# Kernel optimization log

Measured on AMD Instinct MI355X. Metric: run time of the kernel, lower is better.

## Reference

```python
import jax, jax.numpy as jnp
import numpy as np

B, S, D, A = 16, 2048, 512, 512

def setup_inputs() -> dict:
    key = jax.random.key(0)
    ks = jax.random.split(key, 7)
    scale = 1.0 / np.sqrt(D)
    return {
        "query": jax.random.normal(ks[0], (B, S, D), dtype=jnp.float32),
        "key_": jax.random.normal(ks[1], (B, S, D), dtype=jnp.float32),
        "value": jax.random.normal(ks[2], (B, S, D), dtype=jnp.float32),
        "Wq": jax.random.normal(ks[3], (D, A), dtype=jnp.float32) * scale,
        "Wk": jax.random.normal(ks[4], (D, A), dtype=jnp.float32) * scale,
        "Wv": jax.random.normal(ks[5], (D, A), dtype=jnp.float32) * scale,
        "Ws": jax.random.normal(ks[6], (A, 1), dtype=jnp.float32) * (1.0 / np.sqrt(A)),
    }

def reference(query, key_, value, Wq, Wk, Wv, Ws):
    # Dense projections (no bias): [B,S,D] @ [D,A] -> [B,S,A]
    q = jnp.einsum("bsd,da->bsa", query, Wq)
    k = jnp.einsum("bsd,da->bsa", key_, Wk)
    v = jnp.einsum("bsd,da->bsa", value, Wv)
    # Additive (Bahdanau) scores: tanh(q+k) @ Ws -> [B,S]
    scores = jnp.einsum("bsa,a->bs", jnp.tanh(q + k), Ws[:, 0])
    attention_weights = jax.nn.softmax(scores, axis=1)[..., None]  # [B,S,1]
    context_vector = jnp.sum(attention_weights * v, axis=1)        # [B,A]
    return context_vector, attention_weights
```

## Files before the change

kernel.cpp:

```cpp
#include <hip/hip_runtime.h>
#include <hip/hip_bf16.h>
#include <stdint.h>

#define B_ 16
#define S_ 2048
#define D_ 512
#define A_ 512

typedef __attribute__((ext_vector_type(4))) float f32x4;
typedef __attribute__((ext_vector_type(8))) short bf16x8;

__device__ inline unsigned short f2bf(float f) {
  union { float f; unsigned int u; } c; c.f = f;
  unsigned int u = c.u;
  unsigned int r = (u + 0x7fffu + ((u >> 16) & 1u)) >> 16;
  return (unsigned short)r;
}

__device__ inline unsigned pk2bf(float x, float y) {
  __hip_bfloat162 p = __float22bfloat162_rn(float2{x, y});
  union { __hip_bfloat162 h; unsigned u; } c; c.h = p;
  return c.u;
}

__device__ inline float fast_tanh(float x) {
  float e = __expf(2.0f * x);
  return 1.0f - 2.0f * __builtin_amdgcn_rcpf(e + 1.0f);
}

__global__ __launch_bounds__(256) void k0_pack_w(const float* __restrict__ Wq,
                                                 const float* __restrict__ Wk,
                                                 unsigned short* __restrict__ WT) {
  __shared__ unsigned short tile[64][65];
  int bid = blockIdx.x;
  int dt = bid & 15, at = bid >> 4;
  int d0 = dt * 64, a0 = at * 64;
  int t = threadIdx.x;
  int col = t & 63, rbase = t >> 6;
#pragma unroll
  for (int r8 = 0; r8 < 16; ++r8) {
    int row = r8 * 4 + rbase;
    int dcat = d0 + row;
    float f = (dcat < 512) ? Wq[(size_t)dcat * 512 + a0 + col]
                           : Wk[(size_t)(dcat - 512) * 512 + a0 + col];
    tile[row][col] = f2bf(f);
  }
  __syncthreads();
#pragma unroll
  for (int r8 = 0; r8 < 16; ++r8) {
    int arow = r8 * 4 + rbase;
    WT[(size_t)(a0 + arow) * 1024 + d0 + col] = tile[col][arow];
  }
}

__global__ __launch_bounds__(512, 2) void k1_scores(
    const float* __restrict__ Q, const float* __restrict__ K,
    const unsigned short* __restrict__ WT, const float* __restrict__ Wsv,
    float* __restrict__ score) {
  __shared__ unsigned short Al[2][128 * 32];
  __shared__ float scw[8][128];

  const int t = threadIdx.x;
  const int lane = t & 63, w = t >> 6;
  const int frow = lane & 15, fsl = lane >> 4;
  const int row0 = (int)blockIdx.x * 128;

  const int ar = t >> 2, ak = (t & 3) * 8;
  const int abyte = ar * 64 + (((t & 3) ^ ((ar >> 1) & 3)) * 16);

  float4 rA0[2], rA1[2];

  auto issueA = [&](int p, float4* r) {
    const float* src = (p < 16) ? Q : K;
    const float* ap = src + (size_t)(row0 + ar) * 512 + ((p * 32) & 511) + ak;
    r[0] = *(const float4*)(ap);
    r[1] = *(const float4*)(ap + 4);
  };
  auto writeA = [&](const float4* r, int buf) {
    uint4 d;
    d.x = pk2bf(r[0].x, r[0].y);
    d.y = pk2bf(r[0].z, r[0].w);
    d.z = pk2bf(r[1].x, r[1].y);
    d.w = pk2bf(r[1].z, r[1].w);
    *(uint4*)((char*)&Al[buf][0] + abyte) = d;
  };

  const char* bbase = (const char*)WT + (size_t)(w * 64 + frow) * 2048 + fsl * 16;

  f32x4 acc[8][4];
#pragma unroll
  for (int m = 0; m < 8; ++m)
#pragma unroll
    for (int n = 0; n < 4; ++n) acc[m][n] = (f32x4){0.f, 0.f, 0.f, 0.f};

  const int ch = (fsl ^ ((frow >> 1) & 3)) * 16;

  auto doMfma = [&](int p, int CUR) {
    bf16x8 bfr[4];
#pragma unroll
    for (int n = 0; n < 4; ++n)
      bfr[n] = *(const bf16x8*)(bbase + (size_t)n * 16 * 2048 + p * 64);
    bf16x8 af[8];
#pragma unroll
    for (int m = 0; m < 8; ++m)
      af[m] = *(const bf16x8*)((const char*)&Al[CUR][0] + (m * 16 + frow) * 64 + ch);
    __builtin_amdgcn_s_setprio(1);
#pragma unroll
    for (int m = 0; m < 8; ++m)
#pragma unroll
      for (int n = 0; n < 4; ++n)
        acc[m][n] = __builtin_amdgcn_mfma_f32_16x16x32_bf16(af[m], bfr[n], acc[m][n], 0, 0, 0);
    __builtin_amdgcn_s_setprio(0);
  };

  issueA(0, rA0);
  __builtin_amdgcn_sched_barrier(0);
  issueA(1, rA1);
  writeA(rA0, 0);
  asm volatile("s_waitcnt vmcnt(2) lgkmcnt(0)" ::: "memory");
  __builtin_amdgcn_s_barrier();

  auto phase = [&](int p, int CUR, float4* rCur, const float4* rNext) {
    issueA(p + 2, rCur);
    doMfma(p, CUR);
    writeA(rNext, CUR ^ 1);
    asm volatile("s_waitcnt vmcnt(2) lgkmcnt(0)" ::: "memory");
    __builtin_amdgcn_s_barrier();
  };

  for (int kt2 = 0; kt2 < 15; ++kt2) {
    phase(2 * kt2 + 0, 0, rA0, rA1);
    phase(2 * kt2 + 1, 1, rA1, rA0);
  }

  doMfma(30, 0);
  writeA(rA1, 1);
  asm volatile("s_waitcnt vmcnt(0) lgkmcnt(0)" ::: "memory");
  __builtin_amdgcn_s_barrier();
  doMfma(31, 1);

  float wsv[4];
#pragma unroll
  for (int n = 0; n < 4; ++n) wsv[n] = Wsv[w * 64 + n * 16 + frow];
#pragma unroll
  for (int m = 0; m < 8; ++m) {
#pragma unroll
    for (int ii = 0; ii < 4; ++ii) {
      float s = 0.f;
#pragma unroll
      for (int n = 0; n < 4; ++n)
        s += fast_tanh(acc[m][n][ii]) * wsv[n];
      s += __shfl_xor(s, 1);
      s += __shfl_xor(s, 2);
      s += __shfl_xor(s, 4);
      s += __shfl_xor(s, 8);
      if (frow == 0) scw[w][m * 16 + fsl * 4 + ii] = s;
    }
  }
  __syncthreads();
  if (t < 128) {
    float s = 0.f;
#pragma unroll
    for (int ww = 0; ww < 8; ++ww) s += scw[ww][t];
    score[row0 + t] = s;
  }
}

__global__ __launch_bounds__(256) void k3_vsum(const float* __restrict__ value,
                                               const float* __restrict__ score,
                                               float* __restrict__ upart,
                                               float* __restrict__ outw) {
  int bid = blockIdx.x;
  int dh = bid & 1, sc = (bid >> 1) & 15, b = bid >> 5;
  int t = threadIdx.x;
  int lane = t & 63, wave = t >> 6;
  int dg = t & 63, sg = t >> 6;
  __shared__ float red[4], red2[4];
  __shared__ float wl[128];
  __shared__ f32x4 redv[4][64];

  float v[8];
  float mx = -1e30f;
#pragma unroll
  for (int e = 0; e < 8; ++e) {
    float p = score[(size_t)b * S_ + e * 256 + t];
    v[e] = p;
    mx = fmaxf(mx, p);
  }
  for (int off = 1; off < 64; off <<= 1) mx = fmaxf(mx, __shfl_xor(mx, off));
  if (lane == 0) red[wave] = mx;
  __syncthreads();
  mx = fmaxf(fmaxf(red[0], red[1]), fmaxf(red[2], red[3]));
  float sum = 0.f;
#pragma unroll
  for (int e = 0; e < 8; ++e) sum += expf(v[e] - mx);
  for (int off = 1; off < 64; off <<= 1) sum += __shfl_xor(sum, off);
  if (lane == 0) red2[wave] = sum;
  __syncthreads();
  sum = red2[0] + red2[1] + red2[2] + red2[3];
  float inv = 1.f / sum;

  int s0 = sc * 128;
  if (t < 128) {
    size_t o = (size_t)b * S_ + s0 + t;
    float ww = expf(score[o] - mx) * inv;
    wl[t] = ww;
    if (dh == 0) outw[o] = ww;
  }
  __syncthreads();

  const float* vp = value + ((size_t)b * S_ + s0) * 512 + dh * 256 + dg * 4;
  f32x4 a = (f32x4){0.f, 0.f, 0.f, 0.f};
  for (int s = sg; s < 128; s += 4) {
    float4 v4 = *(const float4*)(vp + (size_t)s * 512);
    float ws = wl[s];
    a[0] += ws * v4.x; a[1] += ws * v4.y; a[2] += ws * v4.z; a[3] += ws * v4.w;
  }
  redv[sg][dg] = a;
  __syncthreads();
  if (sg == 0) {
    f32x4 r = redv[0][dg] + redv[1][dg] + redv[2][dg] + redv[3][dg];
    float* dst = upart + (size_t)(sc * 16 + b) * 512 + dh * 256 + dg * 4;
    dst[0] = r[0]; dst[1] = r[1]; dst[2] = r[2]; dst[3] = r[3];
  }
}

__global__ __launch_bounds__(256) void k4_ctx(const float* __restrict__ upart,
                                              const float* __restrict__ Wv,
                                              float* __restrict__ out) {
  int b = blockIdx.x >> 2, q = blockIdx.x & 3;
  int t = threadIdx.x;
  int col = q * 128 + (t & 127), dhf = t >> 7;
  __shared__ float ul[512];
  __shared__ float part[2][128];
  for (int i = t; i < 512; i += 256) {
    float u = 0.f;
#pragma unroll
    for (int c = 0; c < 16; ++c) u += upart[(size_t)(c * 16 + b) * 512 + i];
    ul[i] = u;
  }
  __syncthreads();
  float acc = 0.f;
#pragma unroll 8
  for (int d = dhf * 256; d < dhf * 256 + 256; ++d)
    acc += ul[d] * Wv[(size_t)d * 512 + col];
  part[dhf][t & 127] = acc;
  __syncthreads();
  if (dhf == 0)
    out[(size_t)b * 512 + col] = part[0][t & 127] + part[1][t & 127];
}

extern "C" void kernel_launch(void* const* d_in, const int* in_sizes, int n_in,
                              void* d_out, int out_size, void* d_ws, size_t ws_size,
                              hipStream_t stream) {
  const float* Q  = (const float*)d_in[0];
  const float* Kk = (const float*)d_in[1];
  const float* V  = (const float*)d_in[2];
  const float* Wq = (const float*)d_in[3];
  const float* Wk = (const float*)d_in[4];
  const float* Wv = (const float*)d_in[5];
  const float* Ws = (const float*)d_in[6];
  float* out = (float*)d_out;

  char* ws = (char*)d_ws;
  unsigned short* WT = (unsigned short*)ws;
  float* score = (float*)(ws + (1 << 20));
  float* upart = (float*)(ws + (1 << 20) + (512 << 10));

  float* outw = out + B_ * A_;

  k0_pack_w<<<dim3(128), dim3(256), 0, stream>>>(Wq, Wk, WT);
  k1_scores<<<dim3(256), dim3(512), 0, stream>>>(Q, Kk, WT, Ws, score);
  k3_vsum<<<dim3(512), dim3(256), 0, stream>>>(V, score, upart, outw);
  k4_ctx<<<dim3(64), dim3(256), 0, stream>>>(upart, Wv, out);
}
```

Before: 100.0 us.

## Load A fragments directly from global into registers, drop LDS staging and barriers

The scores GEMM kernel no longer stages the bf16 Q/K tile through double-buffered shared memory with block barriers. Each wave now owns a 64x128 sub-tile (2x4 wave grid) and loads its A fragments straight from global fp32, converting to bf16 in registers, with register double buffering of A and B. This removes LDS traffic and barrier stalls. In exchange each A row is re-read by the four column waves from global/L2, and uncoalesced per-lane loads plus higher register pressure may hurt occupancy.

New measurement: 159.0 us. 59.0% more time.

```diff
diff --git a/kernel.cpp b/kernel.cpp
--- a/kernel.cpp
+++ b/kernel.cpp
@@ -57,112 +57,106 @@
     const float* __restrict__ Q, const float* __restrict__ K,
     const unsigned short* __restrict__ WT, const float* __restrict__ Wsv,
     float* __restrict__ score) {
-  __shared__ unsigned short Al[2][128 * 32];
-  __shared__ float scw[8][128];
+  __shared__ float scw[4][128];
 
   const int t = threadIdx.x;
   const int lane = t & 63, w = t >> 6;
   const int frow = lane & 15, fsl = lane >> 4;
+  const int wr = w >> 2, wc = w & 3;
   const int row0 = (int)blockIdx.x * 128;
 
-  const int ar = t >> 2, ak = (t & 3) * 8;
-  const int abyte = ar * 64 + (((t & 3) ^ ((ar >> 1) & 3)) * 16);
-
-  float4 rA0[2], rA1[2];
-
-  auto issueA = [&](int p, float4* r) {
-    const float* src = (p < 16) ? Q : K;
-    const float* ap = src + (size_t)(row0 + ar) * 512 + ((p * 32) & 511) + ak;
-    r[0] = *(const float4*)(ap);
-    r[1] = *(const float4*)(ap + 4);
-  };
-  auto writeA = [&](const float4* r, int buf) {
-    uint4 d;
-    d.x = pk2bf(r[0].x, r[0].y);
-    d.y = pk2bf(r[0].z, r[0].w);
-    d.z = pk2bf(r[1].x, r[1].y);
-    d.w = pk2bf(r[1].z, r[1].w);
-    *(uint4*)((char*)&Al[buf][0] + abyte) = d;
-  };
-
-  const char* bbase = (const char*)WT + (size_t)(w * 64 + frow) * 2048 + fsl * 16;
-
-  f32x4 acc[8][4];
-#pragma unroll
-  for (int m = 0; m < 8; ++m)
-#pragma unroll
-    for (int n = 0; n < 4; ++n) acc[m][n] = (f32x4){0.f, 0.f, 0.f, 0.f};
-
-  const int ch = (fsl ^ ((frow >> 1) & 3)) * 16;
-
-  auto doMfma = [&](int p, int CUR) {
-    bf16x8 bfr[4];
-#pragma unroll
-    for (int n = 0; n < 4; ++n)
-      bfr[n] = *(const bf16x8*)(bbase + (size_t)n * 16 * 2048 + p * 64);
-    bf16x8 af[8];
-#pragma unroll
-    for (int m = 0; m < 8; ++m)
-      af[m] = *(const bf16x8*)((const char*)&Al[CUR][0] + (m * 16 + frow) * 64 + ch);
+  const float* aQ = Q + (size_t)(row0 + wr * 64 + frow) * 512 + fsl * 8;
+  const float* aK = K + (size_t)(row0 + wr * 64 + frow) * 512 + fsl * 8;
+  const unsigned short* bB = WT + (size_t)(wc * 128 + frow) * 1024 + fsl * 8;
+
+  float4 fa0[4][2], fa1[4][2];
+  bf16x8 a0[4], a1[4], b0[8], b1[8];
+
+  auto loadA = [&](int p, float4 fa[4][2]) {
+    const float* base = (p < 16) ? aQ : aK;
+    const float* ap = base + ((p * 32) & 511);
+#pragma unroll
+    for (int m = 0; m < 4; ++m) {
+      fa[m][0] = *(const float4*)(ap + (size_t)m * 16 * 512);
+      fa[m][1] = *(const float4*)(ap + (size_t)m * 16 * 512 + 4);
+    }
+  };
+  auto cvtA = [&](const float4 fa[4][2], bf16x8* a) {
+#pragma unroll
+    for (int m = 0; m < 4; ++m) {
+      union { bf16x8 v; unsigned u[4]; } c;
+      c.u[0] = pk2bf(fa[m][0].x, fa[m][0].y);
+      c.u[1] = pk2bf(fa[m][0].z, fa[m][0].w);
+      c.u[2] = pk2bf(fa[m][1].x, fa[m][1].y);
+      c.u[3] = pk2bf(fa[m][1].z, fa[m][1].w);
+      a[m] = c.v;
+    }
+  };
+  auto loadB = [&](int p, bf16x8* b) {
+    const unsigned short* bp = bB + p * 32;
+#pragma unroll
+    for (int n = 0; n < 8; ++n)
+      b[n] = *(const bf16x8*)(bp + (size_t)n * 16 * 1024);
+  };
+
+  f32x4 acc[4][8];
+#pragma unroll
+  for (int m = 0; m < 4; ++m)
+#pragma unroll
+    for (int n = 0; n < 8; ++n) acc[m][n] = (f32x4){0.f, 0.f, 0.f, 0.f};
+
+  auto doMfma = [&](const bf16x8* a, const bf16x8* b) {
     __builtin_amdgcn_s_setprio(1);
 #pragma unroll
-    for (int m = 0; m < 8; ++m)
-#pragma unroll
-      for (int n = 0; n < 4; ++n)
-        acc[m][n] = __builtin_amdgcn_mfma_f32_16x16x32_bf16(af[m], bfr[n], acc[m][n], 0, 0, 0);
+    for (int m = 0; m < 4; ++m)
+#pragma unroll
+      for (int n = 0; n < 8; ++n)
+        acc[m][n] = __builtin_amdgcn_mfma_f32_16x16x32_bf16(a[m], b[n], acc[m][n], 0, 0, 0);
     __builtin_amdgcn_s_setprio(0);
   };
 
-  issueA(0, rA0);
-  __builtin_amdgcn_sched_barrier(0);
-  issueA(1, rA1);
-  writeA(rA0, 0);
-  asm volatile("s_waitcnt vmcnt(2) lgkmcnt(0)" ::: "memory");
-  __builtin_amdgcn_s_barrier();
-
-  auto phase = [&](int p, int CUR, float4* rCur, const float4* rNext) {
-    issueA(p + 2, rCur);
-    doMfma(p, CUR);
-    writeA(rNext, CUR ^ 1);
-    asm volatile("s_waitcnt vmcnt(2) lgkmcnt(0)" ::: "memory");
-    __builtin_amdgcn_s_barrier();
-  };
+  loadA(0, fa0);
+  loadB(0, b0);
+  cvtA(fa0, a0);
 
   for (int kt2 = 0; kt2 < 15; ++kt2) {
-    phase(2 * kt2 + 0, 0, rA0, rA1);
-    phase(2 * kt2 + 1, 1, rA1, rA0);
-  }
-
-  doMfma(30, 0);
-  writeA(rA1, 1);
-  asm volatile("s_waitcnt vmcnt(0) lgkmcnt(0)" ::: "memory");
-  __builtin_amdgcn_s_barrier();
-  doMfma(31, 1);
-
-  float wsv[4];
-#pragma unroll
-  for (int n = 0; n < 4; ++n) wsv[n] = Wsv[w * 64 + n * 16 + frow];
-#pragma unroll
-  for (int m = 0; m < 8; ++m) {
+    const int p0 = 2 * kt2, p1 = 2 * kt2 + 1;
+    loadA(p1, fa1);
+    loadB(p1, b1);
+    doMfma(a0, b0);
+    cvtA(fa1, a1);
+    loadA(p1 + 1, fa0);
+    loadB(p1 + 1, b0);
+    doMfma(a1, b1);
+    cvtA(fa0, a0);
+  }
+  loadA(31, fa1);
+  loadB(31, b1);
+  doMfma(a0, b0);
+  cvtA(fa1, a1);
+  doMfma(a1, b1);
+
+  float wsv[8];
+#pragma unroll
+  for (int n = 0; n < 8; ++n) wsv[n] = Wsv[wc * 128 + n * 16 + frow];
+#pragma unroll
+  for (int m = 0; m < 4; ++m) {
 #pragma unroll
     for (int ii = 0; ii < 4; ++ii) {
       float s = 0.f;
 #pragma unroll
-      for (int n = 0; n < 4; ++n)
+      for (int n = 0; n < 8; ++n)
         s += fast_tanh(acc[m][n][ii]) * wsv[n];
       s += __shfl_xor(s, 1);
       s += __shfl_xor(s, 2);
       s += __shfl_xor(s, 4);
       s += __shfl_xor(s, 8);
-      if (frow == 0) scw[w][m * 16 + fsl * 4 + ii] = s;
+      if (frow == 0) scw[wc][wr * 64 + m * 16 + fsl * 4 + ii] = s;
     }
   }
   __syncthreads();
   if (t < 128) {
-    float s = 0.f;
-#pragma unroll
-    for (int ww = 0; ww < 8; ++ww) s += scw[ww][t];
-    score[row0 + t] = s;
+    score[row0 + t] = scw[0][t] + scw[1][t] + scw[2][t] + scw[3][t];
   }
 }
 
```
